# Kernel optimization log

Hardware: AMD Instinct MI355X
Metric: run time of the kernel (lower is better)

Reference implementation:

```python
import jax, jax.numpy as jnp
import numpy as np
import math

B, L, H, E = 4, 1024, 8, 64

def setup_inputs() -> dict:
    key = jax.random.key(0)
    kq, kk, kv, ks = jax.random.split(key, 4)
    return {
        "queries": jax.random.normal(kq, (B, L, H, E), dtype=jnp.float32),
        "keys": jax.random.normal(kk, (B, L, H, E), dtype=jnp.float32),
        "values": jax.random.normal(kv, (B, L, H, E), dtype=jnp.float32),
        "sigma": jax.random.normal(ks, (B, L, H), dtype=jnp.float32),
    }

def reference(queries, keys, values, sigma):
    b, l, h, e = queries.shape
    scale = 1.0 / math.sqrt(e)
    # QK^T scores: [B,H,L,S]
    scores = jnp.einsum('blhe,bshe->bhls', queries, keys)
    # triangular causal mask (mask_flag=True, attn_mask=None path)
    causal = jnp.triu(jnp.ones((l, l), dtype=bool), k=1)
    scores = jnp.where(causal[None, None], -jnp.inf, scores)
    attn = scale * scores
    # sigma -> Gaussian prior
    sig = jnp.transpose(sigma, (0, 2, 1))                      # [B,H,L]
    sig = jax.nn.sigmoid(sig * 5.0) + 1e-5
    sig = jnp.power(3.0, sig) - 1.0
    sig = jnp.broadcast_to(sig[..., None], (b, h, l, l))       # [B,H,L,L]
    idx = jnp.arange(l)
    dist = jnp.abs(idx[:, None] - idx[None, :]).astype(jnp.float32)  # [L,L]
    inv_sqrt_2pi = 1.0 / math.sqrt(2.0 * math.pi)
    prior = inv_sqrt_2pi / sig * jnp.exp(-(dist ** 2) / 2.0 / (sig ** 2))
    series = jax.nn.softmax(attn, axis=-1)                     # dropout p=0 -> identity
    V = jnp.einsum('bhls,bshd->blhd', series, values)
    return V, series, prior, sig
```

## Files before the change

### kernel.cpp

```cpp
#include <hip/hip_runtime.h>

typedef __attribute__((ext_vector_type(8))) short bf16x8;
typedef __attribute__((ext_vector_type(4))) float f32x4;

constexpr int NB = 4, NL = 1024, NH = 8, NE = 64, NBH = NB * NH;

constexpr size_t OFF_V      = 0;
constexpr size_t OFF_SERIES = (size_t)NB * NL * NH * NE;
constexpr size_t OFF_PRIOR  = OFF_SERIES + (size_t)NBH * NL * NL;
constexpr size_t OFF_SIG    = OFF_PRIOR  + (size_t)NBH * NL * NL;

__device__ __forceinline__ unsigned short f2bf(float x) {
  unsigned int u = __builtin_bit_cast(unsigned int, x);
  u = (u + 0x7FFFu + ((u >> 16) & 1u)) >> 16;
  return (unsigned short)u;
}

__device__ __forceinline__ f32x4 mfma16(bf16x8 a, bf16x8 b, f32x4 c) {
  return __builtin_amdgcn_mfma_f32_16x16x32_bf16(a, b, c, 0, 0, 0);
}

__device__ __forceinline__ void loadT(const float* __restrict__ src, float4* r) {
  const int t = threadIdx.x;
  const int s = t >> 2, q = t & 3;
  const float4* rp = (const float4*)(src + (size_t)s * (NH * NE) + q * 16);
  r[0] = rp[0]; r[1] = rp[1]; r[2] = rp[2]; r[3] = rp[3];
}

__device__ __forceinline__ void writeT(const float4* v, unsigned short* lds) {
  const int t = threadIdx.x;
  const int s = t >> 2, q = t & 3;
  unsigned int u[8];
  u[0] = f2bf(v[0].x) | ((unsigned)f2bf(v[0].y) << 16);
  u[1] = f2bf(v[0].z) | ((unsigned)f2bf(v[0].w) << 16);
  u[2] = f2bf(v[1].x) | ((unsigned)f2bf(v[1].y) << 16);
  u[3] = f2bf(v[1].z) | ((unsigned)f2bf(v[1].w) << 16);
  u[4] = f2bf(v[2].x) | ((unsigned)f2bf(v[2].y) << 16);
  u[5] = f2bf(v[2].z) | ((unsigned)f2bf(v[2].w) << 16);
  u[6] = f2bf(v[3].x) | ((unsigned)f2bf(v[3].y) << 16);
  u[7] = f2bf(v[3].z) | ((unsigned)f2bf(v[3].w) << 16);
  const int sw = (s & 7) << 4;
  char* row = (char*)lds + s * 128;
  *(uint4*)(row + ((q * 32)      ^ sw)) = make_uint4(u[0], u[1], u[2], u[3]);
  *(uint4*)(row + ((q * 32 + 16) ^ sw)) = make_uint4(u[4], u[5], u[6], u[7]);
}

__device__ __forceinline__ void loadV(const float* __restrict__ src, float4* r) {
  const int t = threadIdx.x;
  const int sp = t >> 3, ec = t & 7;
  const float* r0 = src + (size_t)(2 * sp) * (NH * NE) + ec * 8;
  const float* r1 = r0 + NH * NE;
  r[0] = ((const float4*)r0)[0]; r[1] = ((const float4*)r0)[1];
  r[2] = ((const float4*)r1)[0]; r[3] = ((const float4*)r1)[1];
}

__device__ __forceinline__ void writeV(const float4* v, unsigned int* ldsv) {
  const int t = threadIdx.x;
  const int sp = t >> 3, ec = t & 7;
  unsigned int u[8];
  u[0] = f2bf(v[0].x) | ((unsigned)f2bf(v[2].x) << 16);
  u[1] = f2bf(v[0].y) | ((unsigned)f2bf(v[2].y) << 16);
  u[2] = f2bf(v[0].z) | ((unsigned)f2bf(v[2].z) << 16);
  u[3] = f2bf(v[0].w) | ((unsigned)f2bf(v[2].w) << 16);
  u[4] = f2bf(v[1].x) | ((unsigned)f2bf(v[3].x) << 16);
  u[5] = f2bf(v[1].y) | ((unsigned)f2bf(v[3].y) << 16);
  u[6] = f2bf(v[1].z) | ((unsigned)f2bf(v[3].z) << 16);
  u[7] = f2bf(v[1].w) | ((unsigned)f2bf(v[3].w) << 16);
  unsigned int* p = ldsv + sp * 68 + ec * 8;
  *(uint4*)(p)     = make_uint4(u[0], u[1], u[2], u[3]);
  *(uint4*)(p + 4) = make_uint4(u[4], u[5], u[6], u[7]);
}

__device__ __forceinline__ void stageQ(const float* __restrict__ src,
                                       unsigned short* lds) {
  float4 r[4];
  loadT(src, r);
  writeT(r, lds);
}

__device__ __forceinline__ bf16x8 readAB(const unsigned short* lds, int row,
                                         int bytecol) {
  const char* p = (const char*)lds + row * 128 + (bytecol ^ ((row & 7) << 4));
  return *(const bf16x8*)p;
}

__global__ __launch_bounds__(256)
void attn_kernel(const float* __restrict__ Qp, const float* __restrict__ Kp,
                 const float* __restrict__ Vp, float* __restrict__ rws,
                 float* __restrict__ out) {
  const int blk = blockIdx.x;
  const int bh = blk & 31;
  const int g5 = blk >> 5;
  const int w  = (g5 < 8) ? (15 - g5) : (g5 - 8);
  const int b = bh >> 3, h = bh & 7;

  __shared__ unsigned short ldsQ[64 * 64];
  __shared__ unsigned short ldsK[64 * 64];
  __shared__ unsigned int   ldsV[32 * 68];
  __shared__ unsigned short ldsP[4][16 * 72];

  const int tid  = threadIdx.x;
  const int lane = tid & 63;
  const int wv   = tid >> 6;
  const int g    = lane >> 4;
  const int e0   = lane & 15;

  const size_t rowstride = NH * NE;
  const float* Qbase = Qp + ((size_t)(b * NL + w * 64) * NH + h) * NE;
  const float* Kbase = Kp + ((size_t)(b * NL) * NH + h) * NE;
  const float* Vbase = Vp + ((size_t)(b * NL) * NH + h) * NE;

  stageQ(Qbase, ldsQ);
  __syncthreads();

  const bf16x8 aq0 = readAB(ldsQ, wv * 16 + e0, g * 16);
  const bf16x8 aq1 = readAB(ldsQ, wv * 16 + e0, g * 16 + 64);

  const float scale = 0.125f;
  const int r_glob0 = w * 64 + wv * 16 + g * 4;
  float rsum[4] = {0.f, 0.f, 0.f, 0.f};

  f32x4 acc_o[4];
#pragma unroll
  for (int i = 0; i < 4; ++i) acc_o[i] = f32x4{0.f, 0.f, 0.f, 0.f};

  unsigned short* ldsPw = ldsP[wv];
  float* __restrict__ series = out + OFF_SERIES + (size_t)bh * NL * NL;

  float4 kreg[4], vreg[4];
  loadT(Kbase, kreg);
  loadV(Vbase, vreg);

  for (int st = 0; st <= w; ++st) {
    __syncthreads();
    writeT(kreg, ldsK);
    writeV(vreg, ldsV);
    __syncthreads();
    if (st < w) {
      loadT(Kbase + (size_t)((st + 1) * 64) * rowstride, kreg);
      loadV(Vbase + (size_t)((st + 1) * 64) * rowstride, vreg);
    }
#pragma unroll
    for (int ct = 0; ct < 4; ++ct) {
      f32x4 acc = {0.f, 0.f, 0.f, 0.f};
      bf16x8 bk0 = readAB(ldsK, ct * 16 + e0, g * 16);
      bf16x8 bk1 = readAB(ldsK, ct * 16 + e0, g * 16 + 64);
      acc = mfma16(aq0, bk0, acc);
      acc = mfma16(aq1, bk1, acc);
      const int s_g = st * 64 + ct * 16 + e0;
#pragma unroll
      for (int j = 0; j < 4; ++j) {
        float e = __expf(acc[j] * scale - 20.0f);
        if (s_g > r_glob0 + j) e = 0.f;
        rsum[j] += e;
        series[(size_t)(r_glob0 + j) * NL + s_g] = e;
        ldsPw[(g * 4 + j) * 72 + ct * 16 + e0] = f2bf(e);
      }
    }
    __builtin_amdgcn_s_setprio(1);
#pragma unroll
    for (int sh = 0; sh < 2; ++sh) {
      const char* pp = (const char*)ldsPw + e0 * 144 + sh * 64 + g * 16;
      const bf16x8 ap = *(const bf16x8*)pp;
#pragma unroll
      for (int ce = 0; ce < 4; ++ce) {
        const unsigned int* vp = ldsV + (sh * 16 + g * 4) * 68 + ce * 16 + e0;
        uint4 vw = make_uint4(vp[0], vp[68], vp[136], vp[204]);
        const bf16x8 bv = __builtin_bit_cast(bf16x8, vw);
        acc_o[ce] = mfma16(ap, bv, acc_o[ce]);
      }
    }
    __builtin_amdgcn_s_setprio(0);
  }

  float rinv[4];
#pragma unroll
  for (int j = 0; j < 4; ++j) {
    float v = rsum[j];
    v += __shfl_xor(v, 1);
    v += __shfl_xor(v, 2);
    v += __shfl_xor(v, 4);
    v += __shfl_xor(v, 8);
    rinv[j] = 1.0f / v;
  }
  if (e0 == 0) {
#pragma unroll
    for (int j = 0; j < 4; ++j) rws[(size_t)bh * NL + r_glob0 + j] = rinv[j];
  }

  float* __restrict__ vout = out + OFF_V;
#pragma unroll
  for (int ce = 0; ce < 4; ++ce) {
#pragma unroll
    for (int j = 0; j < 4; ++j) {
      vout[((size_t)(b * NL + r_glob0 + j) * NH + h) * NE + ce * 16 + e0] =
          acc_o[ce][j] * rinv[j];
    }
  }
}

__global__ __launch_bounds__(256)
void prior_norm_kernel(const float* __restrict__ sigma,
                       const float* __restrict__ rws, float* __restrict__ out) {
  const float inv_sqrt_2pi = 0.39894228040143267f;
  const float ln3 = 1.0986122886681098f;
  float4* __restrict__ prior4  = (float4*)(out + OFF_PRIOR);
  float4* __restrict__ sig4    = (float4*)(out + OFF_SIG);
  float4* __restrict__ series4 = (float4*)(out + OFF_SERIES);

  const int tid  = threadIdx.x;
  const int lane = tid & 63;
  const int rowIdx = blockIdx.x * 4 + (tid >> 6);
  const int l  = rowIdx & 1023;
  const int bh = rowIdx >> 10;
  const int b  = bh >> 3, h = bh & 7;

  const float x    = sigma[((size_t)b * NL + l) * NH + h];
  const float sg   = 1.0f / (1.0f + __expf(-5.0f * x)) + 1e-5f;
  const float sigv = __expf(sg * ln3) - 1.0f;
  const float coef = inv_sqrt_2pi / sigv;
  const float inv2 = -0.5f / (sigv * sigv);
  const float rinv = rws[rowIdx];

  const size_t rbase = (size_t)rowIdx * (NL / 4);
  const int rbe4 = ((l & ~63) + 64) >> 2;
  const float4 zero4 = make_float4(0.f, 0.f, 0.f, 0.f);
  const float4 sv = make_float4(sigv, sigv, sigv, sigv);

#pragma unroll
  for (int k = 0; k < 4; ++k) {
    const int c  = lane + k * 64;
    const int sb = c * 4;
    const int d0 = l - sb, d1 = l - (sb + 1), d2 = l - (sb + 2), d3 = l - (sb + 3);
    float4 pr;
    pr.x = coef * __expf((float)(d0 * d0) * inv2);
    pr.y = coef * __expf((float)(d1 * d1) * inv2);
    pr.z = coef * __expf((float)(d2 * d2) * inv2);
    pr.w = coef * __expf((float)(d3 * d3) * inv2);
    prior4[rbase + c] = pr;
    sig4[rbase + c]   = sv;
    if (c >= rbe4) {
      series4[rbase + c] = zero4;
    } else {
      float4 v = series4[rbase + c];
      v.x *= rinv; v.y *= rinv; v.z *= rinv; v.w *= rinv;
      series4[rbase + c] = v;
    }
  }
}

extern "C" void kernel_launch(void* const* d_in, const int* in_sizes, int n_in,
                              void* d_out, int out_size, void* d_ws, size_t ws_size,
                              hipStream_t stream) {
  const float* Qp = (const float*)d_in[0];
  const float* Kp = (const float*)d_in[1];
  const float* Vp = (const float*)d_in[2];
  const float* Sg = (const float*)d_in[3];
  float* out = (float*)d_out;
  float* rws = (float*)d_ws;

  attn_kernel      <<<dim3(512),          dim3(256), 0, stream>>>(Qp, Kp, Vp, rws, out);
  prior_norm_kernel<<<dim3(NBH * NL / 4), dim3(256), 0, stream>>>(Sg, rws, out);
}
```

Baseline: 460.1 us.

## Split attention KV loop across two blocks and skip negligible prior exponentials

```diff
diff --git a/kernel.cpp b/kernel.cpp
--- a/kernel.cpp
+++ b/kernel.cpp
@@ -9,6 +9,10 @@
 constexpr size_t OFF_SERIES = (size_t)NB * NL * NH * NE;
 constexpr size_t OFF_PRIOR  = OFF_SERIES + (size_t)NBH * NL * NL;
 constexpr size_t OFF_SIG    = OFF_PRIOR  + (size_t)NBH * NL * NL;
+
+constexpr size_t NV = (size_t)NB * NL * NH * NE;
+constexpr size_t WS_SPART   = 2 * NV;
+constexpr size_t WS_FLOATS  = WS_SPART + 2 * (size_t)NBH * NL;
 
 __device__ __forceinline__ unsigned short f2bf(float x) {
   unsigned int u = __builtin_bit_cast(unsigned int, x);
@@ -84,15 +88,20 @@
   return *(const bf16x8*)p;
 }
 
-__global__ __launch_bounds__(256)
+template<bool SPLIT>
+__global__ __launch_bounds__(256, 4)
 void attn_kernel(const float* __restrict__ Qp, const float* __restrict__ Kp,
-                 const float* __restrict__ Vp, float* __restrict__ rws,
+                 const float* __restrict__ Vp, float* __restrict__ ws,
                  float* __restrict__ out) {
   const int blk = blockIdx.x;
   const int bh = blk & 31;
-  const int g5 = blk >> 5;
+  const int g6 = blk >> 5;
+  const int p  = SPLIT ? (g6 >> 4) : 0;
+  const int g5 = g6 & 15;
   const int w  = (g5 < 8) ? (15 - g5) : (g5 - 8);
   const int b = bh >> 3, h = bh & 7;
+  const int start = SPLIT ? p : 0;
+  const int step  = SPLIT ? 2 : 1;
 
   __shared__ unsigned short ldsQ[64 * 64];
   __shared__ unsigned short ldsK[64 * 64];
@@ -128,17 +137,19 @@
   float* __restrict__ series = out + OFF_SERIES + (size_t)bh * NL * NL;
 
   float4 kreg[4], vreg[4];
-  loadT(Kbase, kreg);
-  loadV(Vbase, vreg);
-
-  for (int st = 0; st <= w; ++st) {
+  if (start <= w) {
+    loadT(Kbase + (size_t)(start * 64) * rowstride, kreg);
+    loadV(Vbase + (size_t)(start * 64) * rowstride, vreg);
+  }
+
+  for (int st = start; st <= w; st += step) {
     __syncthreads();
     writeT(kreg, ldsK);
     writeV(vreg, ldsV);
     __syncthreads();
-    if (st < w) {
-      loadT(Kbase + (size_t)((st + 1) * 64) * rowstride, kreg);
-      loadV(Vbase + (size_t)((st + 1) * 64) * rowstride, vreg);
+    if (st + step <= w) {
+      loadT(Kbase + (size_t)((st + step) * 64) * rowstride, kreg);
+      loadV(Vbase + (size_t)((st + step) * 64) * rowstride, vreg);
     }
 #pragma unroll
     for (int ct = 0; ct < 4; ++ct) {
@@ -173,7 +184,7 @@
     __builtin_amdgcn_s_setprio(0);
   }
 
-  float rinv[4];
+  float rred[4];
 #pragma unroll
   for (int j = 0; j < 4; ++j) {
     float v = rsum[j];
@@ -181,27 +192,73 @@
     v += __shfl_xor(v, 2);
     v += __shfl_xor(v, 4);
     v += __shfl_xor(v, 8);
-    rinv[j] = 1.0f / v;
-  }
-  if (e0 == 0) {
-#pragma unroll
-    for (int j = 0; j < 4; ++j) rws[(size_t)bh * NL + r_glob0 + j] = rinv[j];
-  }
-
-  float* __restrict__ vout = out + OFF_V;
-#pragma unroll
-  for (int ce = 0; ce < 4; ++ce) {
-#pragma unroll
-    for (int j = 0; j < 4; ++j) {
-      vout[((size_t)(b * NL + r_glob0 + j) * NH + h) * NE + ce * 16 + e0] =
-          acc_o[ce][j] * rinv[j];
-    }
-  }
+    rred[j] = v;
+  }
+
+  if (SPLIT) {
+    float* spart = ws + WS_SPART + (size_t)p * (NBH * NL);
+    if (e0 == 0) {
+#pragma unroll
+      for (int j = 0; j < 4; ++j) spart[(size_t)bh * NL + r_glob0 + j] = rred[j];
+    }
+    float* vpart = ws + (size_t)p * NV;
+#pragma unroll
+    for (int ce = 0; ce < 4; ++ce) {
+#pragma unroll
+      for (int j = 0; j < 4; ++j) {
+        vpart[((size_t)(b * NL + r_glob0 + j) * NH + h) * NE + ce * 16 + e0] =
+            acc_o[ce][j];
+      }
+    }
+  } else {
+    float* spart0 = ws + WS_SPART;
+    float* spart1 = ws + WS_SPART + (size_t)(NBH * NL);
+    if (e0 == 0) {
+#pragma unroll
+      for (int j = 0; j < 4; ++j) {
+        spart0[(size_t)bh * NL + r_glob0 + j] = rred[j];
+        spart1[(size_t)bh * NL + r_glob0 + j] = 0.f;
+      }
+    }
+    float* __restrict__ vout = out + OFF_V;
+#pragma unroll
+    for (int ce = 0; ce < 4; ++ce) {
+#pragma unroll
+      for (int j = 0; j < 4; ++j) {
+        vout[((size_t)(b * NL + r_glob0 + j) * NH + h) * NE + ce * 16 + e0] =
+            acc_o[ce][j] / rred[j];
+      }
+    }
+  }
+}
+
+__global__ __launch_bounds__(256)
+void vreduce_norm_kernel(const float* __restrict__ ws, float* __restrict__ out) {
+  const size_t idx = (size_t)blockIdx.x * 256 + threadIdx.x;
+  const size_t n4 = NV / 4;
+  const float4* p0 = (const float4*)ws;
+  const float4* p1 = p0 + n4;
+  const size_t flat = idx * 4;
+  const size_t rh   = flat / NE;
+  const size_t h    = rh % NH;
+  const size_t br   = rh / NH;
+  const size_t r    = br % NL;
+  const size_t b    = br / NL;
+  const float* spart = ws + WS_SPART;
+  const size_t so = (b * NH + h) * NL + r;
+  const float inv = 1.0f / (spart[so] + spart[so + NBH * NL]);
+  float4 a = p0[idx], c = p1[idx];
+  float4 o;
+  o.x = (a.x + c.x) * inv;
+  o.y = (a.y + c.y) * inv;
+  o.z = (a.z + c.z) * inv;
+  o.w = (a.w + c.w) * inv;
+  ((float4*)(out + OFF_V))[idx] = o;
 }
 
 __global__ __launch_bounds__(256)
 void prior_norm_kernel(const float* __restrict__ sigma,
-                       const float* __restrict__ rws, float* __restrict__ out) {
+                       const float* __restrict__ ws, float* __restrict__ out) {
   const float inv_sqrt_2pi = 0.39894228040143267f;
   const float ln3 = 1.0986122886681098f;
   float4* __restrict__ prior4  = (float4*)(out + OFF_PRIOR);
@@ -220,7 +277,8 @@
   const float sigv = __expf(sg * ln3) - 1.0f;
   const float coef = inv_sqrt_2pi / sigv;
   const float inv2 = -0.5f / (sigv * sigv);
-  const float rinv = rws[rowIdx];
+  const float* spart = ws + WS_SPART;
+  const float rinv = 1.0f / (spart[rowIdx] + spart[rowIdx + NBH * NL]);
 
   const size_t rbase = (size_t)rowIdx * (NL / 4);
   const int rbe4 = ((l & ~63) + 64) >> 2;
@@ -231,12 +289,15 @@
   for (int k = 0; k < 4; ++k) {
     const int c  = lane + k * 64;
     const int sb = c * 4;
-    const int d0 = l - sb, d1 = l - (sb + 1), d2 = l - (sb + 2), d3 = l - (sb + 3);
-    float4 pr;
-    pr.x = coef * __expf((float)(d0 * d0) * inv2);
-    pr.y = coef * __expf((float)(d1 * d1) * inv2);
-    pr.z = coef * __expf((float)(d2 * d2) * inv2);
-    pr.w = coef * __expf((float)(d3 * d3) * inv2);
+    float4 pr = zero4;
+    const int d = l - sb;
+    if (d <= 135 && d >= -135) {
+      const int d0 = d, d1 = d - 1, d2 = d - 2, d3 = d - 3;
+      pr.x = coef * __expf((float)(d0 * d0) * inv2);
+      pr.y = coef * __expf((float)(d1 * d1) * inv2);
+      pr.z = coef * __expf((float)(d2 * d2) * inv2);
+      pr.w = coef * __expf((float)(d3 * d3) * inv2);
+    }
     prior4[rbase + c] = pr;
     sig4[rbase + c]   = sv;
     if (c >= rbe4) {
@@ -257,8 +318,13 @@
   const float* Vp = (const float*)d_in[2];
   const float* Sg = (const float*)d_in[3];
   float* out = (float*)d_out;
-  float* rws = (float*)d_ws;
-
-  attn_kernel      <<<dim3(512),          dim3(256), 0, stream>>>(Qp, Kp, Vp, rws, out);
-  prior_norm_kernel<<<dim3(NBH * NL / 4), dim3(256), 0, stream>>>(Sg, rws, out);
-}
+  float* ws  = (float*)d_ws;
+
+  if (ws_size >= WS_FLOATS * sizeof(float)) {
+    attn_kernel<true><<<dim3(1024), dim3(256), 0, stream>>>(Qp, Kp, Vp, ws, out);
+    vreduce_norm_kernel<<<dim3(NV / 4 / 256), dim3(256), 0, stream>>>(ws, out);
+  } else {
+    attn_kernel<false><<<dim3(512), dim3(256), 0, stream>>>(Qp, Kp, Vp, ws, out);
+  }
+  prior_norm_kernel<<<dim3(NBH * NL / 4), dim3(256), 0, stream>>>(Sg, ws, out);
+}
```

Result: no change. 467.5 us (+1.6%).
